# Kernel tuning notes

Hardware: AMD Instinct MI355X
Metric: run time of the kernel (lower is better)

## Reference

```python
import jax, jax.numpy as jnp
import numpy as np

WINDOW_SIZE = 128  # matches init_kwargs


def setup_inputs() -> dict:
    key = jax.random.key(0)
    kq, kk, kv = jax.random.split(key, 3)
    B, H, S, D = 1, 8, 2048, 64
    q = jax.random.normal(kq, (B, H, S, D), dtype=jnp.float32)
    k = jax.random.normal(kk, (B, H, S, D), dtype=jnp.float32)
    v = jax.random.normal(kv, (B, H, S, D), dtype=jnp.float32)
    return {"q": q, "k": k, "v": v}


def reference(q, k, v):
    # q, k, v: [B, H, S, D]
    B, H, S, D = q.shape
    w = WINDOW_SIZE // 2  # half-window = 64
    offs = jnp.arange(-w, w + 1)                      # [W] with W = 2w+1 = 129
    pos = jnp.arange(S)[:, None] + offs[None, :]      # [S, W] absolute key index per query
    valid = (pos >= 0) & (pos < S)                    # edge clipping: start=max(0,i-w), end=min(S,i+w+1)
    pos_c = jnp.clip(pos, 0, S - 1)

    # Gather banded keys/values: [B, H, S, W, D]
    k_win = k[:, :, pos_c, :]
    v_win = v[:, :, pos_c, :]

    scale = 1.0 / jnp.sqrt(jnp.asarray(D, dtype=q.dtype))
    scores = jnp.einsum('bhsd,bhswd->bhsw', q, k_win) * scale  # [B, H, S, W]
    neg_inf = jnp.asarray(-jnp.inf, dtype=scores.dtype)
    scores = jnp.where(valid[None, None, :, :], scores, neg_inf)

    attn = jax.nn.softmax(scores, axis=-1)            # every row has >= w+1 valid entries, no NaNs
    out = jnp.einsum('bhsw,bhswd->bhsd', attn, v_win) # [B, H, S, D]
    return out
```

## Files before the change

kernel.cpp:

```cpp
#include <hip/hip_runtime.h>
#include <hip/hip_fp16.h>


#define SEQ 2048
#define QB 64
#define ROWS 192
#define PSTR 40

typedef _Float16 f16x8 __attribute__((ext_vector_type(8)));
typedef float    f32x4 __attribute__((ext_vector_type(4)));

static __device__ __forceinline__ ushort4 pack4(float4 f) {
    union { _Float16 h[4]; ushort4 u; } p;
    p.h[0] = (_Float16)f.x;
    p.h[1] = (_Float16)f.y;
    p.h[2] = (_Float16)f.z;
    p.h[3] = (_Float16)f.w;
    return p.u;
}

__global__ __launch_bounds__(512) void local_attn(
    const float* __restrict__ q,
    const float* __restrict__ k,
    const float* __restrict__ v,
    float* __restrict__ out)
{
    __shared__ __align__(16) _Float16      Kl[ROWS * 72];
    __shared__ __align__(16) unsigned char VtB[64 * 384];
    __shared__ __align__(16) _Float16      Pm[8][16 * PSTR];
    __shared__ __align__(16) float         Cmb[4][64][20];

    const int tid  = threadIdx.x;
    const int lane = tid & 63;
    const int w    = tid >> 6;
    const int t    = w & 3;
    const int half = w >> 2;
    const int l15  = lane & 15;
    const int l4   = lane >> 4;
    const int bx   = blockIdx.x;
    const int h     = bx & 7;
    const int qbase = (bx >> 3) * QB;

    const float* qh = q + (size_t)h * SEQ * 64;
    const float* kh = k + (size_t)h * SEQ * 64;
    const float* vh = v + (size_t)h * SEQ * 64;

    const float* qrow = qh + (size_t)(qbase + t * 16 + l15) * 64 + l4 * 8;
    float4 q0 = *(const float4*)(qrow);
    float4 q1 = *(const float4*)(qrow + 4);
    float4 q2 = *(const float4*)(qrow + 32);
    float4 q3 = *(const float4*)(qrow + 36);

    const int d4  = (tid & 15) << 2;
    const int lr0 = tid >> 4;
    float4 kv[6], vv[6];
    #pragma unroll
    for (int it = 0; it < 6; ++it) {
        int g = qbase - 64 + lr0 + it * 32;
        g = g < 0 ? 0 : (g > SEQ - 1 ? SEQ - 1 : g);
        const float* base = kh + (size_t)g * 64 + d4;
        kv[it] = *(const float4*)(base);
        vv[it] = *(const float4*)(vh + (size_t)g * 64 + d4);
    }

    union uf { f16x8 v; _Float16 hh[8]; };
    uf A0, A1;
    A0.hh[0] = (_Float16)(q0.x * 0.125f); A0.hh[1] = (_Float16)(q0.y * 0.125f);
    A0.hh[2] = (_Float16)(q0.z * 0.125f); A0.hh[3] = (_Float16)(q0.w * 0.125f);
    A0.hh[4] = (_Float16)(q1.x * 0.125f); A0.hh[5] = (_Float16)(q1.y * 0.125f);
    A0.hh[6] = (_Float16)(q1.z * 0.125f); A0.hh[7] = (_Float16)(q1.w * 0.125f);
    A1.hh[0] = (_Float16)(q2.x * 0.125f); A1.hh[1] = (_Float16)(q2.y * 0.125f);
    A1.hh[2] = (_Float16)(q2.z * 0.125f); A1.hh[3] = (_Float16)(q2.w * 0.125f);
    A1.hh[4] = (_Float16)(q3.x * 0.125f); A1.hh[5] = (_Float16)(q3.y * 0.125f);
    A1.hh[6] = (_Float16)(q3.z * 0.125f); A1.hh[7] = (_Float16)(q3.w * 0.125f);

    #pragma unroll
    for (int it = 0; it < 6; ++it) {
        const int lr = lr0 + it * 32;
        *(ushort4*)&Kl[lr * 72 + d4] = pack4(kv[it]);
        #pragma unroll
        for (int i2 = 0; i2 < 4; ++i2) {
            const int d = d4 + i2;
            const int u = (lr >> 3) ^ (d & 7);
            *(_Float16*)&VtB[d * 384 + (u << 4) + (lr & 7) * 2] =
                (_Float16)vv[it][i2];
        }
    }
    __syncthreads();

    _Float16* Pw = Pm[w];
    float rsum[4] = {0.f, 0.f, 0.f, 0.f};
    f32x4 o[4];
    #pragma unroll
    for (int dt = 0; dt < 4; ++dt) o[dt] = (f32x4){0.f, 0.f, 0.f, 0.f};

    #pragma unroll
    for (int c = 0; c < 3; ++c) {
        const int r0 = (half * 3 + c) * 32;

        #pragma unroll
        for (int t2 = 0; t2 < 2; ++t2) {
            const int r = r0 + t2 * 16 + l15;
            f16x8 b0 = *(const f16x8*)&Kl[r * 72 + l4 * 8];
            f16x8 b1 = *(const f16x8*)&Kl[r * 72 + 32 + l4 * 8];
            f32x4 cacc = {0.f, 0.f, 0.f, 0.f};
            cacc = __builtin_amdgcn_mfma_f32_16x16x32_f16(A0.v, b0, cacc, 0, 0, 0);
            cacc = __builtin_amdgcn_mfma_f32_16x16x32_f16(A1.v, b1, cacc, 0, 0, 0);
            const int g  = qbase - 64 + r;
            const bool gv = (g >= 0) & (g < SEQ);
            #pragma unroll
            for (int j = 0; j < 4; ++j) {
                const int qg = qbase + t * 16 + l4 * 4 + j;
                const bool valid = gv && (g >= qg - 64) && (g <= qg + 64);
                const float e = valid ? __expf(cacc[j]) : 0.f;
                rsum[j] += e;
                Pw[(l4 * 4 + j) * PSTR + t2 * 16 + l15] = (_Float16)e;
            }
        }

        asm volatile("s_waitcnt lgkmcnt(0)" ::: "memory");

        f16x8 a = *(const f16x8*)&Pw[l15 * PSTR + l4 * 8];
        #pragma unroll
        for (int dt = 0; dt < 4; ++dt) {
            const int dim = dt * 16 + l15;
            const int u   = ((r0 + l4 * 8) >> 3) ^ (dim & 7);
            f16x8 bb = *(const f16x8*)&VtB[dim * 384 + (u << 4)];
            o[dt] = __builtin_amdgcn_mfma_f32_16x16x32_f16(a, bb, o[dt], 0, 0, 0);
        }
    }

    if (half == 1) {
        #pragma unroll
        for (int dt = 0; dt < 4; ++dt)
            *(f32x4*)&Cmb[t][lane][dt * 4] = o[dt];
        f32x4 pr = {rsum[0], rsum[1], rsum[2], rsum[3]};
        *(f32x4*)&Cmb[t][lane][16] = pr;
    }
    __syncthreads();
    if (half == 0) {
        #pragma unroll
        for (int dt = 0; dt < 4; ++dt) {
            f32x4 p = *(const f32x4*)&Cmb[t][lane][dt * 4];
            o[dt] += p;
        }
        f32x4 pr = *(const f32x4*)&Cmb[t][lane][16];

        #pragma unroll
        for (int j = 0; j < 4; ++j) {
            float l = rsum[j] + pr[j];
            l += __shfl_xor(l, 1, 64);
            l += __shfl_xor(l, 2, 64);
            l += __shfl_xor(l, 4, 64);
            l += __shfl_xor(l, 8, 64);
            const float inv = 1.0f / l;
            const int qg = qbase + t * 16 + l4 * 4 + j;
            #pragma unroll
            for (int dt = 0; dt < 4; ++dt)
                out[((size_t)h * SEQ + qg) * 64 + dt * 16 + l15] = o[dt][j] * inv;
        }
    }
}

extern "C" void kernel_launch(void* const* d_in, const int* in_sizes, int n_in,
                              void* d_out, int out_size, void* d_ws, size_t ws_size,
                              hipStream_t stream)
{
    const float* q = (const float*)d_in[0];
    const float* k = (const float*)d_in[1];
    const float* v = (const float*)d_in[2];
    float* out = (float*)d_out;

    local_attn<<<256, 512, 0, stream>>>(q, k, v, out);
}
```

Baseline: 11.48 us.

## Split key window across three wave groups instead of two per query tile

Raises the block size from 512 to 768 threads so the 192-row key window is split into three 64-row slices, one per group of four waves, with each wave doing two chunks instead of three. Global loads of K/V are spread over more threads (4 loads each instead of 6). Partial outputs and row sums from two groups are combined through a doubled shared-memory buffer. The aim is shorter per-wave critical paths and more latency hiding, at the cost of higher LDS use, a larger reduction, and possibly lower occupancy per CU.

```diff
diff --git a/kernel.cpp b/kernel.cpp
--- a/kernel.cpp
+++ b/kernel.cpp
@@ -19,7 +19,7 @@
     return p.u;
 }
 
-__global__ __launch_bounds__(512) void local_attn(
+__global__ __launch_bounds__(768) void local_attn(
     const float* __restrict__ q,
     const float* __restrict__ k,
     const float* __restrict__ v,
@@ -27,14 +27,14 @@
 {
     __shared__ __align__(16) _Float16      Kl[ROWS * 72];
     __shared__ __align__(16) unsigned char VtB[64 * 384];
-    __shared__ __align__(16) _Float16      Pm[8][16 * PSTR];
-    __shared__ __align__(16) float         Cmb[4][64][20];
+    __shared__ __align__(16) _Float16      Pm[12][16 * PSTR];
+    __shared__ __align__(16) float         Cmb[2][4][64][20];
 
     const int tid  = threadIdx.x;
     const int lane = tid & 63;
     const int w    = tid >> 6;
     const int t    = w & 3;
-    const int half = w >> 2;
+    const int third = w >> 2;
     const int l15  = lane & 15;
     const int l4   = lane >> 4;
     const int bx   = blockIdx.x;
@@ -53,13 +53,12 @@
 
     const int d4  = (tid & 15) << 2;
     const int lr0 = tid >> 4;
-    float4 kv[6], vv[6];
+    float4 kv[4], vv[4];
     #pragma unroll
-    for (int it = 0; it < 6; ++it) {
-        int g = qbase - 64 + lr0 + it * 32;
+    for (int it = 0; it < 4; ++it) {
+        int g = qbase - 64 + lr0 + it * 48;
         g = g < 0 ? 0 : (g > SEQ - 1 ? SEQ - 1 : g);
-        const float* base = kh + (size_t)g * 64 + d4;
-        kv[it] = *(const float4*)(base);
+        kv[it] = *(const float4*)(kh + (size_t)g * 64 + d4);
         vv[it] = *(const float4*)(vh + (size_t)g * 64 + d4);
     }
 
@@ -75,8 +74,8 @@
     A1.hh[6] = (_Float16)(q3.z * 0.125f); A1.hh[7] = (_Float16)(q3.w * 0.125f);
 
     #pragma unroll
-    for (int it = 0; it < 6; ++it) {
-        const int lr = lr0 + it * 32;
+    for (int it = 0; it < 4; ++it) {
+        const int lr = lr0 + it * 48;
         *(ushort4*)&Kl[lr * 72 + d4] = pack4(kv[it]);
         #pragma unroll
         for (int i2 = 0; i2 < 4; ++i2) {
@@ -95,8 +94,8 @@
     for (int dt = 0; dt < 4; ++dt) o[dt] = (f32x4){0.f, 0.f, 0.f, 0.f};
 
     #pragma unroll
-    for (int c = 0; c < 3; ++c) {
-        const int r0 = (half * 3 + c) * 32;
+    for (int c = 0; c < 2; ++c) {
+        const int r0 = (third * 2 + c) * 32;
 
         #pragma unroll
         for (int t2 = 0; t2 < 2; ++t2) {
@@ -130,25 +129,30 @@
         }
     }
 
-    if (half == 1) {
+    if (third > 0) {
+        float* Cl = &Cmb[third - 1][t][lane][0];
         #pragma unroll
         for (int dt = 0; dt < 4; ++dt)
-            *(f32x4*)&Cmb[t][lane][dt * 4] = o[dt];
+            *(f32x4*)(Cl + dt * 4) = o[dt];
         f32x4 pr = {rsum[0], rsum[1], rsum[2], rsum[3]};
-        *(f32x4*)&Cmb[t][lane][16] = pr;
+        *(f32x4*)(Cl + 16) = pr;
     }
     __syncthreads();
-    if (half == 0) {
+    if (third == 0) {
+        const float* C1 = &Cmb[0][t][lane][0];
+        const float* C2 = &Cmb[1][t][lane][0];
         #pragma unroll
         for (int dt = 0; dt < 4; ++dt) {
-            f32x4 p = *(const f32x4*)&Cmb[t][lane][dt * 4];
-            o[dt] += p;
+            f32x4 p1 = *(const f32x4*)(C1 + dt * 4);
+            f32x4 p2 = *(const f32x4*)(C2 + dt * 4);
+            o[dt] += p1 + p2;
         }
-        f32x4 pr = *(const f32x4*)&Cmb[t][lane][16];
+        f32x4 r1 = *(const f32x4*)(C1 + 16);
+        f32x4 r2 = *(const f32x4*)(C2 + 16);
 
         #pragma unroll
         for (int j = 0; j < 4; ++j) {
-            float l = rsum[j] + pr[j];
+            float l = rsum[j] + r1[j] + r2[j];
             l += __shfl_xor(l, 1, 64);
             l += __shfl_xor(l, 2, 64);
             l += __shfl_xor(l, 4, 64);
@@ -171,5 +175,5 @@
     const float* v = (const float*)d_in[2];
     float* out = (float*)d_out;
 
-    local_attn<<<256, 512, 0, stream>>>(q, k, v, out);
+    local_attn<<<256, 768, 0, stream>>>(q, k, v, out);
 }
```

After: 11.57 us. About the same (+0.8%).
